# Kernel tuning notes

Measured on AMD Instinct MI355X. Metric: run time of the kernel, lower is better.

The kernel has to match this reference:

```python
import jax, jax.numpy as jnp
import numpy as np

T, B, N, E = 16384, 64, 1_000_000, 4096  # steps, per-step batch, train samples, eval dim


def setup_inputs() -> dict:
    key = jax.random.key(0)
    k1, k2, k3 = jax.random.split(key, 3)
    indices = jax.random.randint(k1, (T, B), 0, N, dtype=jnp.int64)
    M_prev = jax.random.normal(k2, (E,), dtype=jnp.float32)
    # torch module initializes params to zeros; use small random values so the
    # affine recurrence exercises nontrivial math without blowing up.
    params = jax.random.normal(k3, (N, 2), dtype=jnp.float32) * 0.01
    return {"indices": indices, "M_prev": M_prev, "params": params}


def reference(indices, M_prev, params):
    # Per-step gather + sum: alpha_t = sum(params[idx_t, 0]), beta_t = sum(params[idx_t, 1])
    coeffs = params[indices].sum(axis=1)          # [T, 2]
    alpha, beta = coeffs[:, 0], coeffs[:, 1]      # [T], [T]

    # Affine recurrence M_t = alpha_t * M_{t-1} + beta_t as a parallel scan:
    # compose (a1,b1) then (a2,b2) -> (a2*a1, a2*b1 + b2)
    def compose(c1, c2):
        a1, b1 = c1
        a2, b2 = c2
        return a2 * a1, a2 * b1 + b2

    A, Bc = jax.lax.associative_scan(compose, (alpha, beta))  # prefix affine maps
    # M_t = A_t * M_0 + B_t, broadcast over eval dim -> [T, E]
    return A[:, None] * M_prev[None, :] + Bc[:, None]
```

## Files before the change

kernel.cpp:

```cpp
#include <hip/hip_runtime.h>

#define T_DIM 16384
#define B_DIM 64
#define E_DIM 4096

__global__ __launch_bounds__(256) void coeff_kernel(const int* __restrict__ indices,
                                                    const float* __restrict__ params,
                                                    float* __restrict__ alpha,
                                                    float* __restrict__ beta) {
    int gid = blockIdx.x * blockDim.x + threadIdx.x;
    int t = gid >> 6;
    int lane = threadIdx.x & 63;
    int idx = indices[gid];
    float2 p = ((const float2*)params)[idx];
    float a = p.x, b = p.y;
    #pragma unroll
    for (int off = 32; off >= 1; off >>= 1) {
        a += __shfl_down(a, off, 64);
        b += __shfl_down(b, off, 64);
    }
    if (lane == 0) { alpha[t] = a; beta[t] = b; }
}

__global__ __launch_bounds__(1024) void scan_kernel(const float* __restrict__ alpha,
                                                    const float* __restrict__ beta,
                                                    float* __restrict__ A,
                                                    float* __restrict__ Bc) {
    __shared__ float sA[1024];
    __shared__ float sB[1024];
    const int tid = threadIdx.x;
    const int base = tid * 16;

    float la[16], lb[16];
    float a = 1.0f, b = 0.0f;
    #pragma unroll
    for (int j = 0; j < 16; ++j) {
        float aj = alpha[base + j];
        float bj = beta[base + j];
        a = aj * a;
        b = aj * b + bj;
        la[j] = a; lb[j] = b;
    }
    sA[tid] = a; sB[tid] = b;
    __syncthreads();

    for (int off = 1; off < 1024; off <<= 1) {
        float pa = 1.0f, pb = 0.0f;
        float ca = sA[tid], cb = sB[tid];
        if (tid >= off) { pa = sA[tid - off]; pb = sB[tid - off]; }
        __syncthreads();
        sA[tid] = ca * pa;
        sB[tid] = ca * pb + cb;
        __syncthreads();
    }

    float pa = 1.0f, pb = 0.0f;
    if (tid > 0) { pa = sA[tid - 1]; pb = sB[tid - 1]; }
    #pragma unroll
    for (int j = 0; j < 16; ++j) {
        A[base + j]  = la[j] * pa;
        Bc[base + j] = la[j] * pb + lb[j];
    }
}

__global__ __launch_bounds__(256) void out_kernel(const float* __restrict__ A,
                                                  const float* __restrict__ Bc,
                                                  const float* __restrict__ M,
                                                  float* __restrict__ out) {
    const int t = blockIdx.x;
    const float a = A[t];
    const float b = Bc[t];
    const float4* __restrict__ M4 = (const float4*)M;
    float4* __restrict__ O4 = (float4*)(out + (size_t)t * E_DIM);
    const int tid = threadIdx.x;
    #pragma unroll
    for (int k = 0; k < 4; ++k) {
        int e4 = tid + k * 256;
        float4 m = M4[e4];
        float4 r;
        r.x = a * m.x + b;
        r.y = a * m.y + b;
        r.z = a * m.z + b;
        r.w = a * m.w + b;
        O4[e4] = r;
    }
}

extern "C" void kernel_launch(void* const* d_in, const int* in_sizes, int n_in,
                              void* d_out, int out_size, void* d_ws, size_t ws_size,
                              hipStream_t stream) {
    const int*   indices = (const int*)d_in[0];
    const float* M_prev  = (const float*)d_in[1];
    const float* params  = (const float*)d_in[2];
    float* out = (float*)d_out;

    float* ws    = (float*)d_ws;
    float* alpha = ws;
    float* beta  = ws + T_DIM;
    float* A     = ws + 2 * T_DIM;
    float* Bc    = ws + 3 * T_DIM;

    coeff_kernel<<<(T_DIM * B_DIM) / 256, 256, 0, stream>>>(indices, params, alpha, beta);
    scan_kernel<<<1, 1024, 0, stream>>>(alpha, beta, A, Bc);
    out_kernel<<<T_DIM, 256, 0, stream>>>(A, Bc, M_prev, out);
}
```

Measured before the change: 294.5 us.

## Interleave coefficients, use wave-shuffle scan, multi-row output blocks with nontemporal stores

Coefficients and prefix maps are now stored interleaved as float2 so they can be read and written with vector loads. The single-block scan replaces its shared-memory Hillis-Steele loop, which synchronized at every step, with wave-level shuffle scans plus a small cross-wave aggregate. The output kernel handles eight rows per block, keeps M_prev in registers across those rows, and writes with nontemporal stores. Together these aim to cut scan latency and output-write overhead, at the cost of fewer output blocks.

```diff
diff --git a/kernel.cpp b/kernel.cpp
--- a/kernel.cpp
+++ b/kernel.cpp
@@ -4,10 +4,11 @@
 #define B_DIM 64
 #define E_DIM 4096
 
+typedef float f4 __attribute__((ext_vector_type(4)));
+
 __global__ __launch_bounds__(256) void coeff_kernel(const int* __restrict__ indices,
                                                     const float* __restrict__ params,
-                                                    float* __restrict__ alpha,
-                                                    float* __restrict__ beta) {
+                                                    float2* __restrict__ coeff) {
     int gid = blockIdx.x * blockDim.x + threadIdx.x;
     int t = gid >> 6;
     int lane = threadIdx.x & 63;
@@ -19,70 +20,91 @@
         a += __shfl_down(a, off, 64);
         b += __shfl_down(b, off, 64);
     }
-    if (lane == 0) { alpha[t] = a; beta[t] = b; }
+    if (lane == 0) coeff[t] = make_float2(a, b);
 }
 
-__global__ __launch_bounds__(1024) void scan_kernel(const float* __restrict__ alpha,
-                                                    const float* __restrict__ beta,
-                                                    float* __restrict__ A,
-                                                    float* __restrict__ Bc) {
-    __shared__ float sA[1024];
-    __shared__ float sB[1024];
-    const int tid = threadIdx.x;
+__global__ __launch_bounds__(1024) void scan_kernel(const float2* __restrict__ coeff,
+                                                    float2* __restrict__ AB) {
+    __shared__ float2 wagg[16];
+    const int tid  = threadIdx.x;
+    const int lane = tid & 63;
+    const int w    = tid >> 6;
     const int base = tid * 16;
 
     float la[16], lb[16];
     float a = 1.0f, b = 0.0f;
+    const f4* __restrict__ c4 = (const f4*)(coeff + base);
     #pragma unroll
-    for (int j = 0; j < 16; ++j) {
-        float aj = alpha[base + j];
-        float bj = beta[base + j];
-        a = aj * a;
-        b = aj * b + bj;
-        la[j] = a; lb[j] = b;
+    for (int j4 = 0; j4 < 8; ++j4) {
+        f4 c = c4[j4];
+        a = c.x * a; b = c.x * b + c.y; la[2*j4]   = a; lb[2*j4]   = b;
+        a = c.z * a; b = c.z * b + c.w; la[2*j4+1] = a; lb[2*j4+1] = b;
     }
-    sA[tid] = a; sB[tid] = b;
+
+    #pragma unroll
+    for (int off = 1; off < 64; off <<= 1) {
+        float pa = __shfl_up(a, off, 64);
+        float pb = __shfl_up(b, off, 64);
+        if (lane >= off) { b = a * pb + b; a = a * pa; }
+    }
+    if (lane == 63) wagg[w] = make_float2(a, b);
     __syncthreads();
 
-    for (int off = 1; off < 1024; off <<= 1) {
-        float pa = 1.0f, pb = 0.0f;
-        float ca = sA[tid], cb = sB[tid];
-        if (tid >= off) { pa = sA[tid - off]; pb = sB[tid - off]; }
-        __syncthreads();
-        sA[tid] = ca * pa;
-        sB[tid] = ca * pb + cb;
-        __syncthreads();
+    if (w == 0 && lane < 16) {
+        float wa = wagg[lane].x, wb = wagg[lane].y;
+        #pragma unroll
+        for (int off = 1; off < 16; off <<= 1) {
+            float pa = __shfl_up(wa, off, 64);
+            float pb = __shfl_up(wb, off, 64);
+            if (lane >= off) { wb = wa * pb + wb; wa = wa * pa; }
+        }
+        wagg[lane] = make_float2(wa, wb);
     }
+    __syncthreads();
 
-    float pa = 1.0f, pb = 0.0f;
-    if (tid > 0) { pa = sA[tid - 1]; pb = sB[tid - 1]; }
+    float ea = __shfl_up(a, 1, 64);
+    float eb = __shfl_up(b, 1, 64);
+    if (lane == 0) { ea = 1.0f; eb = 0.0f; }
+    float wa = 1.0f, wb = 0.0f;
+    if (w > 0) { wa = wagg[w - 1].x; wb = wagg[w - 1].y; }
+    float Pa = ea * wa;
+    float Pb = ea * wb + eb;
+
+    f4* __restrict__ o4 = (f4*)(AB + base);
     #pragma unroll
-    for (int j = 0; j < 16; ++j) {
-        A[base + j]  = la[j] * pa;
-        Bc[base + j] = la[j] * pb + lb[j];
+    for (int j4 = 0; j4 < 8; ++j4) {
+        f4 r;
+        r.x = la[2*j4]   * Pa;  r.y = la[2*j4]   * Pb + lb[2*j4];
+        r.z = la[2*j4+1] * Pa;  r.w = la[2*j4+1] * Pb + lb[2*j4+1];
+        o4[j4] = r;
     }
 }
 
-__global__ __launch_bounds__(256) void out_kernel(const float* __restrict__ A,
-                                                  const float* __restrict__ Bc,
+#define ROWS_PER_BLOCK 8
+__global__ __launch_bounds__(256) void out_kernel(const float2* __restrict__ AB,
                                                   const float* __restrict__ M,
                                                   float* __restrict__ out) {
-    const int t = blockIdx.x;
-    const float a = A[t];
-    const float b = Bc[t];
-    const float4* __restrict__ M4 = (const float4*)M;
-    float4* __restrict__ O4 = (float4*)(out + (size_t)t * E_DIM);
+    const int t0  = blockIdx.x * ROWS_PER_BLOCK;
     const int tid = threadIdx.x;
+    const f4* __restrict__ M4 = (const f4*)M;
+    f4 m0 = M4[tid];
+    f4 m1 = M4[tid + 256];
+    f4 m2 = M4[tid + 512];
+    f4 m3 = M4[tid + 768];
     #pragma unroll
-    for (int k = 0; k < 4; ++k) {
-        int e4 = tid + k * 256;
-        float4 m = M4[e4];
-        float4 r;
-        r.x = a * m.x + b;
-        r.y = a * m.y + b;
-        r.z = a * m.z + b;
-        r.w = a * m.w + b;
-        O4[e4] = r;
+    for (int r = 0; r < ROWS_PER_BLOCK; ++r) {
+        const int t = t0 + r;
+        float2 ab = AB[t];
+        const float a = ab.x, b = ab.y;
+        f4* __restrict__ O4 = (f4*)(out + (size_t)t * E_DIM);
+        f4 v0 = { a * m0.x + b, a * m0.y + b, a * m0.z + b, a * m0.w + b };
+        f4 v1 = { a * m1.x + b, a * m1.y + b, a * m1.z + b, a * m1.w + b };
+        f4 v2 = { a * m2.x + b, a * m2.y + b, a * m2.z + b, a * m2.w + b };
+        f4 v3 = { a * m3.x + b, a * m3.y + b, a * m3.z + b, a * m3.w + b };
+        __builtin_nontemporal_store(v0, O4 + tid);
+        __builtin_nontemporal_store(v1, O4 + tid + 256);
+        __builtin_nontemporal_store(v2, O4 + tid + 512);
+        __builtin_nontemporal_store(v3, O4 + tid + 768);
     }
 }
 
@@ -94,13 +116,10 @@
     const float* params  = (const float*)d_in[2];
     float* out = (float*)d_out;
 
-    float* ws    = (float*)d_ws;
-    float* alpha = ws;
-    float* beta  = ws + T_DIM;
-    float* A     = ws + 2 * T_DIM;
-    float* Bc    = ws + 3 * T_DIM;
+    float2* coeff = (float2*)d_ws;
+    float2* AB    = ((float2*)d_ws) + T_DIM;
 
-    coeff_kernel<<<(T_DIM * B_DIM) / 256, 256, 0, stream>>>(indices, params, alpha, beta);
-    scan_kernel<<<1, 1024, 0, stream>>>(alpha, beta, A, Bc);
-    out_kernel<<<T_DIM, 256, 0, stream>>>(A, Bc, M_prev, out);
+    coeff_kernel<<<(T_DIM * B_DIM) / 256, 256, 0, stream>>>(indices, params, coeff);
+    scan_kernel<<<1, 1024, 0, stream>>>(coeff, AB);
+    out_kernel<<<T_DIM / ROWS_PER_BLOCK, 256, 0, stream>>>(AB, M_prev, out);
 }
```

Result: no change. 299.3 us (+1.6%).
